# Kernel optimization log

Measured on AMD Instinct MI355X. Metric: run time of the kernel, lower is better.

## Reference

```python
import jax, jax.numpy as jnp
import numpy as np

B, N, NF, ND, NH = 16, 128, 64, 100, 64

def glorot(key, shape):
    fan_in, fan_out = shape[0], shape[1]
    limit = np.sqrt(6.0 / (fan_in + fan_out)).astype(np.float32)
    return jax.random.uniform(key, shape, jnp.float32, -limit, limit)

def setup_inputs() -> dict:
    key = jax.random.key(0)
    k1, k2, k3, k4, k5 = jax.random.split(key, 5)
    return {
        "atom_features": jax.random.normal(k1, (B, N, NF), jnp.float32),
        "distance_matrix": jax.random.uniform(k2, (B, N, N, ND), jnp.float32),
        "distance_matrix_mask": jnp.ones((B, N, N), jnp.float32),
        "W_cf": glorot(k3, (NF, NH)),
        "W_df": glorot(k4, (ND, NH)),
        "W_fc": glorot(k5, (NH, NF)),
        "b_cf": jnp.zeros((NH,), jnp.float32),
        "b_df": jnp.zeros((NH,), jnp.float32),
    }

def reference(atom_features, distance_matrix, distance_matrix_mask, W_cf, W_df, W_fc, b_cf, b_df):
    # dist_h: [B, N, N, H]
    dist_h = jnp.einsum('bijd,dh->bijh', distance_matrix, W_df) + b_df
    # atom_h: [B, N, H] -> broadcast over axis 1 (matches tf expand_dims axis=1)
    atom_h = jnp.einsum('bjf,fh->bjh', atom_features, W_cf) + b_cf
    gated = dist_h * atom_h[:, None, :, :]                 # [B, N, N, H]
    out = jnp.einsum('bijh,hf->bijf', gated, W_fc)          # [B, N, N, F]
    out = out * distance_matrix_mask[..., None]
    out = jnp.tanh(out)
    return jnp.sum(out, axis=2) + atom_features             # [B, N, F]
```

## Files before the change

kernel.cpp:

```cpp
#include <hip/hip_runtime.h>
#include <hip/hip_bf16.h>

#define Bsz 16
#define Nn  128
#define NFd 64
#define NDd 100
#define NHd 64

typedef __attribute__((ext_vector_type(8))) short bf16x8;
typedef __attribute__((ext_vector_type(4))) float f32x4;

__device__ __forceinline__ short f2bf(float f) {
  return (short)__builtin_bit_cast(ushort, __float2bfloat16(f));
}

__device__ __forceinline__ float fast_tanh(float x) {
  float e = __expf(2.0f * x);
  return 1.0f - 2.0f * __builtin_amdgcn_rcpf(e + 1.0f);
}

__device__ __forceinline__ void glds16(const float* g, float* l) {
  __builtin_amdgcn_global_load_lds(
      (const __attribute__((address_space(1))) void*)g,
      (__attribute__((address_space(3))) void*)l, 16, 0, 0);
}
__device__ __forceinline__ void glds4(const float* g, float* l) {
  __builtin_amdgcn_global_load_lds(
      (const __attribute__((address_space(1))) void*)g,
      (__attribute__((address_space(3))) void*)l, 4, 0, 0);
}

__global__ __launch_bounds__(256) void prep_kernel(
    const float* __restrict__ AF, const float* __restrict__ Wcf,
    const float* __restrict__ bcf, const float* __restrict__ Wdf,
    const float* __restrict__ Wfc, float* __restrict__ atomh,
    ushort* __restrict__ wdfp, ushort* __restrict__ wfcp) {
  int t = threadIdx.x;
  int blk = blockIdx.x;
  if (blk < 512) {
    int row = blk * 4 + (t >> 6);
    int h = t & 63;
    const float* af = AF + (size_t)row * NFd;
    float a0 = 0.f, a1 = 0.f, a2 = 0.f, a3 = 0.f;
    #pragma unroll 4
    for (int f = 0; f < NFd; f += 4) {
      a0 += af[f + 0] * Wcf[(f + 0) * NHd + h];
      a1 += af[f + 1] * Wcf[(f + 1) * NHd + h];
      a2 += af[f + 2] * Wcf[(f + 2) * NHd + h];
      a3 += af[f + 3] * Wcf[(f + 3) * NHd + h];
    }
    atomh[(size_t)row * NHd + h] = bcf[h] + ((a0 + a1) + (a2 + a3));
  } else if (blk < 544) {
    int idx = (blk - 512) * 256 + t;
    int e = idx & 7;
    int col = (idx >> 3) & 63;
    int grp = idx >> 9;
    int k = grp * 8 + e;
    float v = (k < NDd) ? Wdf[k * NHd + col] : 0.f;
    wdfp[idx] = (ushort)f2bf(v);
  } else {
    int idx = (blk - 544) * 256 + t;
    int e = idx & 7;
    int col = (idx >> 3) & 63;
    int grp = idx >> 9;
    int k = grp * 8 + e;
    wfcp[idx] = (ushort)f2bf(Wfc[k * NFd + col]);
  }
}

__global__ __launch_bounds__(256, 3) void dtnn_main_kernel(
    const float* __restrict__ AF,
    const float* __restrict__ DM,
    const float* __restrict__ MASK,
    const float* __restrict__ bdf,
    const float* __restrict__ atomh,
    const ushort* __restrict__ wdfp,
    const ushort* __restrict__ wfcp,
    float* __restrict__ out) {
  __shared__ float stage[12832];
  __shared__ float red[256];

  const int t    = threadIdx.x;
  const int bi   = blockIdx.x;
  const int b    = bi >> 7;
  const int w    = t >> 6;
  const int lane = t & 63;
  const int p    = t & 15;
  const int q    = (t >> 4) & 3;

  const float* gsrc = DM + (size_t)bi * (Nn * NDd) + w * 3200;
  float* lbase = stage + w * 3200;
  #pragma unroll
  for (int v = 0; v < 12; ++v)
    glds16(gsrc + v * 256 + lane * 4, lbase + v * 256);
  glds4(gsrc + 3072 + lane, lbase + 3072);
  glds4(gsrc + 3136 + lane, lbase + 3136);

  asm volatile("s_waitcnt vmcnt(0)" ::: "memory");
  __builtin_amdgcn_sched_barrier(0);

  const bf16x8* wdfv = reinterpret_cast<const bf16x8*>(wdfp);
  const bf16x8* wfcv = reinterpret_cast<const bf16x8*>(wfcp);

  float s[4] = {0.f, 0.f, 0.f, 0.f};

  #pragma unroll 1
  for (int jt = 0; jt < 2; ++jt) {
    const int jrow = (2 * w + jt) * 16;

    f32x4 acc[4];
    #pragma unroll
    for (int ht = 0; ht < 4; ++ht) {
      float bv = bdf[ht * 16 + p];
      acc[ht] = (f32x4){bv, bv, bv, bv};
    }

    const float* arow = stage + (jrow + p) * 100;
    #pragma unroll
    for (int ks = 0; ks < 4; ++ks) {
      float4 x = *reinterpret_cast<const float4*>(arow + ks * 32 + q * 8);
      float4 y = *reinterpret_cast<const float4*>(arow + ks * 32 + q * 8 + 4);
      bf16x8 a;
      a[0] = f2bf(x.x); a[1] = f2bf(x.y); a[2] = f2bf(x.z); a[3] = f2bf(x.w);
      a[4] = f2bf(y.x); a[5] = f2bf(y.y); a[6] = f2bf(y.z); a[7] = f2bf(y.w);
      #pragma unroll
      for (int ht = 0; ht < 4; ++ht)
        acc[ht] = __builtin_amdgcn_mfma_f32_16x16x32_bf16(
            a, wdfv[(ks * 4 + q) * 64 + ht * 16 + p], acc[ht], 0, 0, 0);
    }

    const float* ap = atomh + ((size_t)(b * Nn + jrow + 4 * q)) * NHd + p;
    #pragma unroll
    for (int ht = 0; ht < 4; ++ht) {
      #pragma unroll
      for (int r = 0; r < 4; ++r) acc[ht][r] *= ap[r * NHd + ht * 16];
    }

    ushort* gb = reinterpret_cast<ushort*>(stage + w * 3200 + jt * 1600);
    #pragma unroll
    for (int r = 0; r < 4; ++r) {
      int rr = 4 * q + r;
      int sw = (rr & 7) << 3;
      #pragma unroll
      for (int ht = 0; ht < 4; ++ht)
        gb[rr * 64 + ((ht * 16 + p) ^ sw)] = (ushort)f2bf(acc[ht][r]);
    }
    asm volatile("" ::: "memory");

    f32x4 acc2[4];
    #pragma unroll
    for (int ft = 0; ft < 4; ++ft) acc2[ft] = (f32x4){0.f, 0.f, 0.f, 0.f};

    #pragma unroll
    for (int ks = 0; ks < 2; ++ks) {
      int h0 = (ks * 32 + q * 8) ^ ((p & 7) << 3);
      bf16x8 a2 = *reinterpret_cast<const bf16x8*>(&gb[p * 64 + h0]);
      #pragma unroll
      for (int ft = 0; ft < 4; ++ft)
        acc2[ft] = __builtin_amdgcn_mfma_f32_16x16x32_bf16(
            a2, wfcv[(ks * 4 + q) * 64 + ft * 16 + p], acc2[ft], 0, 0, 0);
    }

    #pragma unroll
    for (int r = 0; r < 4; ++r) {
      float m = MASK[(size_t)bi * Nn + jrow + 4 * q + r];
      #pragma unroll
      for (int ft = 0; ft < 4; ++ft) s[ft] += fast_tanh(acc2[ft][r] * m);
    }
  }

  #pragma unroll
  for (int ft = 0; ft < 4; ++ft) {
    s[ft] += __shfl_xor(s[ft], 16, 64);
    s[ft] += __shfl_xor(s[ft], 32, 64);
  }
  if (q == 0) {
    #pragma unroll
    for (int ft = 0; ft < 4; ++ft) red[w * 64 + ft * 16 + p] = s[ft];
  }
  __syncthreads();
  if (t < 64) {
    float tot = red[t] + red[64 + t] + red[128 + t] + red[192 + t];
    out[(size_t)bi * NFd + t] = tot + AF[(size_t)bi * NFd + t];
  }
}

extern "C" void kernel_launch(void* const* d_in, const int* in_sizes, int n_in,
                              void* d_out, int out_size, void* d_ws, size_t ws_size,
                              hipStream_t stream) {
  const float* AF   = (const float*)d_in[0];
  const float* DM   = (const float*)d_in[1];
  const float* MASK = (const float*)d_in[2];
  const float* Wcf  = (const float*)d_in[3];
  const float* Wdf  = (const float*)d_in[4];
  const float* Wfc  = (const float*)d_in[5];
  const float* bcf  = (const float*)d_in[6];
  const float* bdf  = (const float*)d_in[7];
  float* out = (float*)d_out;

  float*  atomh = (float*)d_ws;
  ushort* wdfp  = (ushort*)((char*)d_ws + 524288);
  ushort* wfcp  = (ushort*)((char*)d_ws + 524288 + 16384);

  prep_kernel<<<560, 256, 0, stream>>>(AF, Wcf, bcf, Wdf, Wfc, atomh, wdfp, wfcp);
  dtnn_main_kernel<<<Bsz * Nn, 256, 0, stream>>>(AF, DM, MASK, bdf, atomh, wdfp, wfcp, out);
}
```

Measured before the change: 41.06 us.

## Split each row across two blocks with atomic output accumulation

Each output row is now handled by two blocks of 64 j-rows each instead of one block of 128, which halves the LDS staging and raises the occupancy target from 3 to 6 blocks per CU. The residual copy of atom_features into out moves into the prep kernel, and the main kernel accumulates partial sums straight into global memory with atomic adds instead of an LDS reduction and __syncthreads. The K loop for the first GEMM now uses 3 full steps plus a partial one, skipping padded zero work. In exchange it adds global atomics, float summation order that is no longer fixed, and a dependency on prep having initialised out.

```diff
diff --git a/kernel.cpp b/kernel.cpp
--- a/kernel.cpp
+++ b/kernel.cpp
@@ -34,7 +34,8 @@
     const float* __restrict__ AF, const float* __restrict__ Wcf,
     const float* __restrict__ bcf, const float* __restrict__ Wdf,
     const float* __restrict__ Wfc, float* __restrict__ atomh,
-    ushort* __restrict__ wdfp, ushort* __restrict__ wfcp) {
+    ushort* __restrict__ wdfp, ushort* __restrict__ wfcp,
+    float* __restrict__ out) {
   int t = threadIdx.x;
   int blk = blockIdx.x;
   if (blk < 512) {
@@ -58,18 +59,20 @@
     int k = grp * 8 + e;
     float v = (k < NDd) ? Wdf[k * NHd + col] : 0.f;
     wdfp[idx] = (ushort)f2bf(v);
-  } else {
+  } else if (blk < 560) {
     int idx = (blk - 544) * 256 + t;
     int e = idx & 7;
     int col = (idx >> 3) & 63;
     int grp = idx >> 9;
     int k = grp * 8 + e;
     wfcp[idx] = (ushort)f2bf(Wfc[k * NFd + col]);
-  }
-}
-
-__global__ __launch_bounds__(256, 3) void dtnn_main_kernel(
-    const float* __restrict__ AF,
+  } else {
+    int idx = (blk - 560) * 256 + t;
+    out[idx] = AF[idx];
+  }
+}
+
+__global__ __launch_bounds__(256, 6) void dtnn_main_kernel(
     const float* __restrict__ DM,
     const float* __restrict__ MASK,
     const float* __restrict__ bdf,
@@ -77,24 +80,26 @@
     const ushort* __restrict__ wdfp,
     const ushort* __restrict__ wfcp,
     float* __restrict__ out) {
-  __shared__ float stage[12832];
-  __shared__ float red[256];
+  __shared__ float stage[64 * 100];
 
   const int t    = threadIdx.x;
-  const int bi   = blockIdx.x;
+  const int blk  = blockIdx.x;
+  const int bi   = blk >> 1;
+  const int half = blk & 1;
   const int b    = bi >> 7;
   const int w    = t >> 6;
   const int lane = t & 63;
   const int p    = t & 15;
   const int q    = (t >> 4) & 3;
 
-  const float* gsrc = DM + (size_t)bi * (Nn * NDd) + w * 3200;
-  float* lbase = stage + w * 3200;
-  #pragma unroll
-  for (int v = 0; v < 12; ++v)
+  const int jrow = half * 64 + w * 16;
+
+  const float* gsrc = DM + (size_t)bi * (Nn * NDd) + (size_t)jrow * NDd;
+  float* lbase = stage + w * 1600;
+  #pragma unroll
+  for (int v = 0; v < 6; ++v)
     glds16(gsrc + v * 256 + lane * 4, lbase + v * 256);
-  glds4(gsrc + 3072 + lane, lbase + 3072);
-  glds4(gsrc + 3136 + lane, lbase + 3136);
+  glds4(gsrc + 1536 + lane, lbase + 1536);
 
   asm volatile("s_waitcnt vmcnt(0)" ::: "memory");
   __builtin_amdgcn_sched_barrier(0);
@@ -102,71 +107,76 @@
   const bf16x8* wdfv = reinterpret_cast<const bf16x8*>(wdfp);
   const bf16x8* wfcv = reinterpret_cast<const bf16x8*>(wfcp);
 
+  f32x4 acc[4];
+  #pragma unroll
+  for (int ht = 0; ht < 4; ++ht) {
+    float bv = bdf[ht * 16 + p];
+    acc[ht] = (f32x4){bv, bv, bv, bv};
+  }
+
+  const float* arow = stage + (w * 16 + p) * 100;
+  #pragma unroll
+  for (int ks = 0; ks < 3; ++ks) {
+    float4 x = *reinterpret_cast<const float4*>(arow + ks * 32 + q * 8);
+    float4 y = *reinterpret_cast<const float4*>(arow + ks * 32 + q * 8 + 4);
+    bf16x8 a;
+    a[0] = f2bf(x.x); a[1] = f2bf(x.y); a[2] = f2bf(x.z); a[3] = f2bf(x.w);
+    a[4] = f2bf(y.x); a[5] = f2bf(y.y); a[6] = f2bf(y.z); a[7] = f2bf(y.w);
+    #pragma unroll
+    for (int ht = 0; ht < 4; ++ht)
+      acc[ht] = __builtin_amdgcn_mfma_f32_16x16x32_bf16(
+          a, wdfv[(ks * 4 + q) * 64 + ht * 16 + p], acc[ht], 0, 0, 0);
+  }
+  {
+    bf16x8 a = (bf16x8){0, 0, 0, 0, 0, 0, 0, 0};
+    if (q == 0) {
+      float4 x = *reinterpret_cast<const float4*>(arow + 96);
+      a[0] = f2bf(x.x); a[1] = f2bf(x.y); a[2] = f2bf(x.z); a[3] = f2bf(x.w);
+    }
+    #pragma unroll
+    for (int ht = 0; ht < 4; ++ht)
+      acc[ht] = __builtin_amdgcn_mfma_f32_16x16x32_bf16(
+          a, wdfv[(12 + q) * 64 + ht * 16 + p], acc[ht], 0, 0, 0);
+  }
+
+  const float* ap = atomh + ((size_t)(b * Nn + jrow + 4 * q)) * NHd + p;
+  #pragma unroll
+  for (int ht = 0; ht < 4; ++ht) {
+    #pragma unroll
+    for (int r = 0; r < 4; ++r) acc[ht][r] *= ap[r * NHd + ht * 16];
+  }
+
+  ushort* gb = reinterpret_cast<ushort*>(lbase);
+  #pragma unroll
+  for (int r = 0; r < 4; ++r) {
+    int rr = 4 * q + r;
+    int sw = (rr & 7) << 3;
+    #pragma unroll
+    for (int ht = 0; ht < 4; ++ht)
+      gb[rr * 64 + ((ht * 16 + p) ^ sw)] = (ushort)f2bf(acc[ht][r]);
+  }
+  asm volatile("" ::: "memory");
+
+  f32x4 acc2[4];
+  #pragma unroll
+  for (int ft = 0; ft < 4; ++ft) acc2[ft] = (f32x4){0.f, 0.f, 0.f, 0.f};
+
+  #pragma unroll
+  for (int ks = 0; ks < 2; ++ks) {
+    int h0 = (ks * 32 + q * 8) ^ ((p & 7) << 3);
+    bf16x8 a2 = *reinterpret_cast<const bf16x8*>(&gb[p * 64 + h0]);
+    #pragma unroll
+    for (int ft = 0; ft < 4; ++ft)
+      acc2[ft] = __builtin_amdgcn_mfma_f32_16x16x32_bf16(
+          a2, wfcv[(ks * 4 + q) * 64 + ft * 16 + p], acc2[ft], 0, 0, 0);
+  }
+
   float s[4] = {0.f, 0.f, 0.f, 0.f};
-
-  #pragma unroll 1
-  for (int jt = 0; jt < 2; ++jt) {
-    const int jrow = (2 * w + jt) * 16;
-
-    f32x4 acc[4];
-    #pragma unroll
-    for (int ht = 0; ht < 4; ++ht) {
-      float bv = bdf[ht * 16 + p];
-      acc[ht] = (f32x4){bv, bv, bv, bv};
-    }
-
-    const float* arow = stage + (jrow + p) * 100;
-    #pragma unroll
-    for (int ks = 0; ks < 4; ++ks) {
-      float4 x = *reinterpret_cast<const float4*>(arow + ks * 32 + q * 8);
-      float4 y = *reinterpret_cast<const float4*>(arow + ks * 32 + q * 8 + 4);
-      bf16x8 a;
-      a[0] = f2bf(x.x); a[1] = f2bf(x.y); a[2] = f2bf(x.z); a[3] = f2bf(x.w);
-      a[4] = f2bf(y.x); a[5] = f2bf(y.y); a[6] = f2bf(y.z); a[7] = f2bf(y.w);
-      #pragma unroll
-      for (int ht = 0; ht < 4; ++ht)
-        acc[ht] = __builtin_amdgcn_mfma_f32_16x16x32_bf16(
-            a, wdfv[(ks * 4 + q) * 64 + ht * 16 + p], acc[ht], 0, 0, 0);
-    }
-
-    const float* ap = atomh + ((size_t)(b * Nn + jrow + 4 * q)) * NHd + p;
-    #pragma unroll
-    for (int ht = 0; ht < 4; ++ht) {
-      #pragma unroll
-      for (int r = 0; r < 4; ++r) acc[ht][r] *= ap[r * NHd + ht * 16];
-    }
-
-    ushort* gb = reinterpret_cast<ushort*>(stage + w * 3200 + jt * 1600);
-    #pragma unroll
-    for (int r = 0; r < 4; ++r) {
-      int rr = 4 * q + r;
-      int sw = (rr & 7) << 3;
-      #pragma unroll
-      for (int ht = 0; ht < 4; ++ht)
-        gb[rr * 64 + ((ht * 16 + p) ^ sw)] = (ushort)f2bf(acc[ht][r]);
-    }
-    asm volatile("" ::: "memory");
-
-    f32x4 acc2[4];
-    #pragma unroll
-    for (int ft = 0; ft < 4; ++ft) acc2[ft] = (f32x4){0.f, 0.f, 0.f, 0.f};
-
-    #pragma unroll
-    for (int ks = 0; ks < 2; ++ks) {
-      int h0 = (ks * 32 + q * 8) ^ ((p & 7) << 3);
-      bf16x8 a2 = *reinterpret_cast<const bf16x8*>(&gb[p * 64 + h0]);
-      #pragma unroll
-      for (int ft = 0; ft < 4; ++ft)
-        acc2[ft] = __builtin_amdgcn_mfma_f32_16x16x32_bf16(
-            a2, wfcv[(ks * 4 + q) * 64 + ft * 16 + p], acc2[ft], 0, 0, 0);
-    }
-
-    #pragma unroll
-    for (int r = 0; r < 4; ++r) {
-      float m = MASK[(size_t)bi * Nn + jrow + 4 * q + r];
-      #pragma unroll
-      for (int ft = 0; ft < 4; ++ft) s[ft] += fast_tanh(acc2[ft][r] * m);
-    }
+  #pragma unroll
+  for (int r = 0; r < 4; ++r) {
+    float m = MASK[(size_t)bi * Nn + jrow + 4 * q + r];
+    #pragma unroll
+    for (int ft = 0; ft < 4; ++ft) s[ft] += fast_tanh(acc2[ft][r] * m);
   }
 
   #pragma unroll
@@ -176,12 +186,8 @@
   }
   if (q == 0) {
     #pragma unroll
-    for (int ft = 0; ft < 4; ++ft) red[w * 64 + ft * 16 + p] = s[ft];
-  }
-  __syncthreads();
-  if (t < 64) {
-    float tot = red[t] + red[64 + t] + red[128 + t] + red[192 + t];
-    out[(size_t)bi * NFd + t] = tot + AF[(size_t)bi * NFd + t];
+    for (int ft = 0; ft < 4; ++ft)
+      unsafeAtomicAdd(&out[(size_t)bi * NFd + ft * 16 + p], s[ft]);
   }
 }
 
@@ -202,6 +208,6 @@
   ushort* wdfp  = (ushort*)((char*)d_ws + 524288);
   ushort* wfcp  = (ushort*)((char*)d_ws + 524288 + 16384);
 
-  prep_kernel<<<560, 256, 0, stream>>>(AF, Wcf, bcf, Wdf, Wfc, atomh, wdfp, wfcp);
-  dtnn_main_kernel<<<Bsz * Nn, 256, 0, stream>>>(AF, DM, MASK, bdf, atomh, wdfp, wfcp, out);
-}
+  prep_kernel<<<1072, 256, 0, stream>>>(AF, Wcf, bcf, Wdf, Wfc, atomh, wdfp, wfcp, out);
+  dtnn_main_kernel<<<2 * Bsz * Nn, 256, 0, stream>>>(DM, MASK, bdf, atomh, wdfp, wfcp, out);
+}
```

After: 35.84 us. 12.7% less time.
